# Kernel optimization log

Hardware: AMD Instinct MI355X
Metric: run time of the kernel (lower is better)

The kernel has to match this reference:

```python
import jax, jax.numpy as jnp
from jax import lax
import numpy as np

INPUT, HIDDEN, OUTPUT, SEQ = 1024, 1024, 1024, 8192


def setup_inputs() -> dict:
    key = jax.random.key(0)
    ks = jax.random.split(key, 7)
    s = 1.0 / np.sqrt(HIDDEN)
    return {
        "input_seq": jax.random.normal(ks[0], (SEQ, INPUT), dtype=jnp.float32),
        # PyTorch nn.LSTM params, gate order [i, f, g, o]
        "W_ih": jax.random.uniform(ks[1], (4 * HIDDEN, INPUT), jnp.float32, -s, s),
        "W_hh": jax.random.uniform(ks[2], (4 * HIDDEN, HIDDEN), jnp.float32, -s, s),
        "b_ih": jax.random.uniform(ks[3], (4 * HIDDEN,), jnp.float32, -s, s),
        "b_hh": jax.random.uniform(ks[4], (4 * HIDDEN,), jnp.float32, -s, s),
        "W_out": jax.random.uniform(ks[5], (OUTPUT, HIDDEN), jnp.float32, -s, s),
        "b_out": jax.random.uniform(ks[6], (OUTPUT,), jnp.float32, -s, s),
    }


def reference(input_seq, W_ih, W_hh, b_ih, b_hh, W_out, b_out):
    H = W_hh.shape[1]
    # Precompute input projections for all timesteps in one GEMM: [S, 4H]
    x_gates = input_seq @ W_ih.T + (b_ih + b_hh)

    def step(carry, xg):
        h, c = carry
        gates = xg + h @ W_hh.T                      # [4H]
        i = jax.nn.sigmoid(gates[:H])
        f = jax.nn.sigmoid(gates[H:2 * H])
        g = jnp.tanh(gates[2 * H:3 * H])
        o = jax.nn.sigmoid(gates[3 * H:])
        c = f * c + i * g
        h = o * jnp.tanh(c)
        return (h, c), None

    h0 = jnp.zeros((H,), dtype=input_seq.dtype)
    (h_final, _), _ = lax.scan(step, (h0, h0), x_gates)
    # Original applies linear per-timestep then takes predictions[-1];
    # linear is pointwise in time, so projecting only h_final is identical math.
    return h_final @ W_out.T + b_out
```

## Files before the change

kernel.cpp:

```cpp
#include <hip/hip_runtime.h>
#include <hip/hip_fp16.h>

typedef _Float16 h2v __attribute__((ext_vector_type(2)));

__device__ __forceinline__ float fdot2(unsigned int a, unsigned int b, float c) {
    return __builtin_amdgcn_fdot2(__builtin_bit_cast(h2v, a),
                                  __builtin_bit_cast(h2v, b), c, false);
}

#define SCOPE_AGENT __HIP_MEMORY_SCOPE_AGENT

__global__ __launch_bounds__(256) void k_f2h(const float* __restrict__ src,
                                             __half* __restrict__ dst, int n4) {
    int i = blockIdx.x * 256 + threadIdx.x;
    if (i >= n4) return;
    float4 v = ((const float4*)src)[i];
    union { __half2 h[2]; uint2 u; } o;
    o.h[0] = __halves2half2(__float2half_rn(v.x), __float2half_rn(v.y));
    o.h[1] = __halves2half2(__float2half_rn(v.z), __float2half_rn(v.w));
    ((uint2*)dst)[i] = o.u;
}

__global__ __launch_bounds__(256) void k_bias(const float* __restrict__ a,
                                              const float* __restrict__ b,
                                              float* __restrict__ o) {
    int i = blockIdx.x * 256 + threadIdx.x;
    if (i < 4096) o[i] = a[i] + b[i];
}

__global__ __launch_bounds__(256) void k_gemm_xg(const __half* __restrict__ A,
                                                 const __half* __restrict__ B,
                                                 const float* __restrict__ bias,
                                                 __half* __restrict__ C) {
    __shared__ unsigned int As[128][20];
    __shared__ unsigned int Bs[128][20];
    const int tid = threadIdx.x;
    const int tx = tid & 15, ty = tid >> 4;
    const int m0 = blockIdx.x * 128, n0 = blockIdx.y * 128;
    float acc[8][8];
#pragma unroll
    for (int i = 0; i < 8; ++i)
#pragma unroll
        for (int j = 0; j < 8; ++j) acc[i][j] = 0.f;
    const unsigned int* Ag = (const unsigned int*)(A + (size_t)m0 * 1024);
    const unsigned int* Bg = (const unsigned int*)(B + (size_t)n0 * 1024);
    for (int k0 = 0; k0 < 512; k0 += 16) {
        __syncthreads();
#pragma unroll
        for (int j = 0; j < 2; ++j) {
            int qd = j * 256 + tid;
            int row = qd >> 2;
            int c4 = (qd & 3) << 2;
            uint4 va = *(const uint4*)(Ag + (size_t)row * 512 + k0 + c4);
            uint4 vb = *(const uint4*)(Bg + (size_t)row * 512 + k0 + c4);
            *(uint4*)&As[row][c4] = va;
            *(uint4*)&Bs[row][c4] = vb;
        }
        __syncthreads();
#pragma unroll
        for (int k2 = 0; k2 < 16; k2 += 2) {
            unsigned int a0[8], a1[8], b0[8], b1[8];
#pragma unroll
            for (int i = 0; i < 8; ++i) {
                uint2 v = *(const uint2*)&As[ty + 16 * i][k2];
                a0[i] = v.x; a1[i] = v.y;
            }
#pragma unroll
            for (int j = 0; j < 8; ++j) {
                uint2 v = *(const uint2*)&Bs[tx + 16 * j][k2];
                b0[j] = v.x; b1[j] = v.y;
            }
#pragma unroll
            for (int i = 0; i < 8; ++i)
#pragma unroll
                for (int j = 0; j < 8; ++j) {
                    acc[i][j] = fdot2(a0[i], b0[j], acc[i][j]);
                    acc[i][j] = fdot2(a1[i], b1[j], acc[i][j]);
                }
        }
    }
#pragma unroll
    for (int i = 0; i < 8; ++i) {
        int row = m0 + ty + 16 * i;
#pragma unroll
        for (int j = 0; j < 8; ++j) {
            int col = n0 + tx + 16 * j;
            C[(size_t)row * 4096 + col] = __float2half_rn(acc[i][j] + bias[col]);
        }
    }
}

__global__ __launch_bounds__(512, 1) void k_lstm(const __half* __restrict__ Whh,
                                                 const __half* __restrict__ xg,
                                                 unsigned long long* pub) {
    __shared__ unsigned int hs[2][544];
    const int tid = threadIdx.x;
    const int b = blockIdx.x;
    const int w = tid >> 6, lane = tid & 63;
    const int rho = lane >> 2;
    const int cc = lane & 3;
    const int grow = (rho & 3) * 1024 + b * 32 + 4 * w + (rho >> 2);
    uint4 wr[32];
#pragma unroll
    for (int i = 0; i < 32; ++i)
        wr[i] = *(const uint4*)(Whh + (size_t)grow * 1024 + cc * 256 + i * 8);
    const int soff = (tid >> 6) * 68 + (tid & 63);
    float c_state = 0.f;
    __syncthreads();

    for (int t = 0; t < 8192; ++t) {
        float xv = __half2float(xg[(size_t)t * 4096 + grow]);
        unsigned int d = 0;
        if (t > 0) {
            const unsigned long long* src = pub + (((t - 1) & 1) << 9);
            unsigned long long v = __hip_atomic_load(src + tid, __ATOMIC_RELAXED, SCOPE_AGENT);
            while ((unsigned)(v >> 32) != (unsigned)t) {
                __builtin_amdgcn_s_sleep(1);
                v = __hip_atomic_load(src + tid, __ATOMIC_RELAXED, SCOPE_AGENT);
            }
            d = (unsigned)v;
        }
        const int p = t & 1;
        hs[p][soff] = d;
        __syncthreads();
        float acc = 0.f;
        const unsigned int* hsp = &hs[p][cc * 136];
#pragma unroll
        for (int i = 0; i < 32; ++i) {
            uint4 h4 = *(const uint4*)(hsp + (i >> 4) * 68 + ((i & 15) << 2));
            acc = fdot2(wr[i].x, h4.x, acc);
            acc = fdot2(wr[i].y, h4.y, acc);
            acc = fdot2(wr[i].z, h4.z, acc);
            acc = fdot2(wr[i].w, h4.w, acc);
        }
        acc += __shfl_xor(acc, 1);
        acc += __shfl_xor(acc, 2);
        acc += xv;
        const int base = lane & 48;
        float gi = __shfl(acc, base + 0);
        float gf = __shfl(acc, base + 4);
        float gg = __shfl(acc, base + 8);
        float go = __shfl(acc, base + 12);
        gi = 1.f / (1.f + __expf(-gi));
        gf = 1.f / (1.f + __expf(-gf));
        gg = 2.f / (1.f + __expf(-2.f * gg)) - 1.f;
        go = 1.f / (1.f + __expf(-go));
        c_state = gf * c_state + gi * gg;
        float hval = go * (2.f / (1.f + __expf(-2.f * c_state)) - 1.f);
        float ha = __shfl(hval, (lane & 1) << 5);
        float hb = __shfl(hval, ((lane & 1) << 5) + 16);
        if (lane < 2) {
            union { __half2 h; unsigned int u; } pk;
            pk.h = __halves2half2(__float2half_rn(ha), __float2half_rn(hb));
            unsigned long long val =
                ((unsigned long long)(unsigned)(t + 1) << 32) | pk.u;
            __hip_atomic_store(pub + (p << 9) + b * 16 + w * 2 + lane, val,
                               __ATOMIC_RELAXED, SCOPE_AGENT);
        }
    }
}

__global__ __launch_bounds__(256) void k_proj(unsigned long long* __restrict__ hfin,
                                              const float* __restrict__ Wout,
                                              const float* __restrict__ bout,
                                              float* __restrict__ out) {
    __shared__ float red[256];
    const int o = blockIdx.x, tid = threadIdx.x;
    const float* wr = Wout + (size_t)o * 1024;
    float acc = 0.f;
#pragma unroll
    for (int j = 0; j < 2; ++j) {
        int e = j * 256 + tid;
        unsigned long long v = __hip_atomic_load(hfin + e, __ATOMIC_RELAXED, SCOPE_AGENT);
        union { unsigned int u; __half2 h; } pk; pk.u = (unsigned)v;
        acc += __half2float(__low2half(pk.h)) * wr[2 * e] +
               __half2float(__high2half(pk.h)) * wr[2 * e + 1];
    }
    red[tid] = acc;
    __syncthreads();
    for (int s = 128; s > 0; s >>= 1) {
        if (tid < s) red[tid] += red[tid + s];
        __syncthreads();
    }
    if (tid == 0) out[o] = red[0] + bout[o];
}

extern "C" void kernel_launch(void* const* d_in, const int* in_sizes, int n_in,
                              void* d_out, int out_size, void* d_ws, size_t ws_size,
                              hipStream_t stream) {
    const float* input_seq = (const float*)d_in[0];
    const float* W_ih = (const float*)d_in[1];
    const float* W_hh = (const float*)d_in[2];
    const float* b_ih = (const float*)d_in[3];
    const float* b_hh = (const float*)d_in[4];
    const float* W_out = (const float*)d_in[5];
    const float* b_out = (const float*)d_in[6];
    float* out = (float*)d_out;

    char* ws = (char*)d_ws;
    unsigned long long* pub = (unsigned long long*)ws;
    float* bias = (float*)(ws + 24576);
    __half* Wih_h = (__half*)(ws + 65536);
    __half* Whh_h = (__half*)(ws + 65536 + (size_t)8 * 1024 * 1024);
    __half* in_h  = (__half*)(ws + 65536 + (size_t)16 * 1024 * 1024);
    __half* xg    = (__half*)(ws + 65536 + (size_t)32 * 1024 * 1024);

    hipMemsetAsync(ws, 0, 8192, stream);

    k_f2h<<<8192, 256, 0, stream>>>(input_seq, in_h, 2 * 1024 * 1024);
    k_f2h<<<4096, 256, 0, stream>>>(W_ih, Wih_h, 1024 * 1024);
    k_f2h<<<4096, 256, 0, stream>>>(W_hh, Whh_h, 1024 * 1024);
    k_bias<<<16, 256, 0, stream>>>(b_ih, b_hh, bias);

    dim3 gg(64, 32);
    k_gemm_xg<<<gg, 256, 0, stream>>>(in_h, Wih_h, bias, xg);

    k_lstm<<<32, 512, 0, stream>>>(Whh_h, xg, pub);

    k_proj<<<1024, 256, 0, stream>>>(pub + 512, W_out, b_out, out);
}
```

Baseline: 20.88 ms.

## Publish each hidden value as a 16-bit tag plus half word, drop sleep

Each hidden value now goes out as a 32-bit word holding a 16-bit timestep tag and one fp16 value. Four lanes per wave publish directly, which removes the cross-lane shuffles before the store. Readers poll 64-bit pairs and check both tags, and the s_sleep in the spin loop is gone. This is meant to cut publish latency on the serial recurrence critical path. In exchange it uses system-scope atomics, which may cost more per access, and the 16-bit tag wraps at 65536, which is still safe for 8192 steps.

After: 20.70 ms. No clear change (-0.9%).

```diff
diff --git a/kernel.cpp b/kernel.cpp
--- a/kernel.cpp
+++ b/kernel.cpp
@@ -8,7 +8,7 @@
                                   __builtin_bit_cast(h2v, b), c, false);
 }
 
-#define SCOPE_AGENT __HIP_MEMORY_SCOPE_AGENT
+#define SCOPE_SYS __HIP_MEMORY_SCOPE_SYSTEM
 
 __global__ __launch_bounds__(256) void k_f2h(const float* __restrict__ src,
                                              __half* __restrict__ dst, int n4) {
@@ -92,7 +92,7 @@
 
 __global__ __launch_bounds__(512, 1) void k_lstm(const __half* __restrict__ Whh,
                                                  const __half* __restrict__ xg,
-                                                 unsigned long long* pub) {
+                                                 unsigned int* pub) {
     __shared__ unsigned int hs[2][544];
     const int tid = threadIdx.x;
     const int b = blockIdx.x;
@@ -105,6 +105,7 @@
     for (int i = 0; i < 32; ++i)
         wr[i] = *(const uint4*)(Whh + (size_t)grow * 1024 + cc * 256 + i * 8);
     const int soff = (tid >> 6) * 68 + (tid & 63);
+    const int upub = b * 32 + w * 4 + (lane >> 4);
     float c_state = 0.f;
     __syncthreads();
 
@@ -112,13 +113,16 @@
         float xv = __half2float(xg[(size_t)t * 4096 + grow]);
         unsigned int d = 0;
         if (t > 0) {
-            const unsigned long long* src = pub + (((t - 1) & 1) << 9);
-            unsigned long long v = __hip_atomic_load(src + tid, __ATOMIC_RELAXED, SCOPE_AGENT);
-            while ((unsigned)(v >> 32) != (unsigned)t) {
-                __builtin_amdgcn_s_sleep(1);
-                v = __hip_atomic_load(src + tid, __ATOMIC_RELAXED, SCOPE_AGENT);
+            const unsigned long long* src =
+                (const unsigned long long*)(pub + (((t - 1) & 1) << 10)) + tid;
+            const unsigned tt = (unsigned)t;
+            unsigned long long v = __hip_atomic_load(src, __ATOMIC_RELAXED, SCOPE_SYS);
+            unsigned lo = (unsigned)v, hi = (unsigned)(v >> 32);
+            while ((lo >> 16) != tt || (hi >> 16) != tt) {
+                v = __hip_atomic_load(src, __ATOMIC_RELAXED, SCOPE_SYS);
+                lo = (unsigned)v; hi = (unsigned)(v >> 32);
             }
-            d = (unsigned)v;
+            d = (lo & 0xffffu) | (hi << 16);
         }
         const int p = t & 1;
         hs[p][soff] = d;
@@ -147,20 +151,16 @@
         go = 1.f / (1.f + __expf(-go));
         c_state = gf * c_state + gi * gg;
         float hval = go * (2.f / (1.f + __expf(-2.f * c_state)) - 1.f);
-        float ha = __shfl(hval, (lane & 1) << 5);
-        float hb = __shfl(hval, ((lane & 1) << 5) + 16);
-        if (lane < 2) {
-            union { __half2 h; unsigned int u; } pk;
-            pk.h = __halves2half2(__float2half_rn(ha), __float2half_rn(hb));
-            unsigned long long val =
-                ((unsigned long long)(unsigned)(t + 1) << 32) | pk.u;
-            __hip_atomic_store(pub + (p << 9) + b * 16 + w * 2 + lane, val,
-                               __ATOMIC_RELAXED, SCOPE_AGENT);
-        }
-    }
-}
-
-__global__ __launch_bounds__(256) void k_proj(unsigned long long* __restrict__ hfin,
+        if ((lane & 15) == 0) {
+            unsigned val = ((unsigned)(t + 1) << 16) |
+                           (unsigned)__half_as_ushort(__float2half_rn(hval));
+            __hip_atomic_store(pub + (p << 10) + upub, val,
+                               __ATOMIC_RELAXED, SCOPE_SYS);
+        }
+    }
+}
+
+__global__ __launch_bounds__(256) void k_proj(const unsigned int* __restrict__ hfin,
                                               const float* __restrict__ Wout,
                                               const float* __restrict__ bout,
                                               float* __restrict__ out) {
@@ -169,12 +169,10 @@
     const float* wr = Wout + (size_t)o * 1024;
     float acc = 0.f;
 #pragma unroll
-    for (int j = 0; j < 2; ++j) {
+    for (int j = 0; j < 4; ++j) {
         int e = j * 256 + tid;
-        unsigned long long v = __hip_atomic_load(hfin + e, __ATOMIC_RELAXED, SCOPE_AGENT);
-        union { unsigned int u; __half2 h; } pk; pk.u = (unsigned)v;
-        acc += __half2float(__low2half(pk.h)) * wr[2 * e] +
-               __half2float(__high2half(pk.h)) * wr[2 * e + 1];
+        unsigned v = hfin[e];
+        acc += __half2float(__ushort_as_half((unsigned short)(v & 0xffffu))) * wr[e];
     }
     red[tid] = acc;
     __syncthreads();
@@ -198,7 +196,7 @@
     float* out = (float*)d_out;
 
     char* ws = (char*)d_ws;
-    unsigned long long* pub = (unsigned long long*)ws;
+    unsigned int* pub = (unsigned int*)ws;
     float* bias = (float*)(ws + 24576);
     __half* Wih_h = (__half*)(ws + 65536);
     __half* Whh_h = (__half*)(ws + 65536 + (size_t)8 * 1024 * 1024);
@@ -217,5 +215,5 @@
 
     k_lstm<<<32, 512, 0, stream>>>(Whh_h, xg, pub);
 
-    k_proj<<<1024, 256, 0, stream>>>(pub + 512, W_out, b_out, out);
-}
+    k_proj<<<1024, 256, 0, stream>>>(pub + 1024, W_out, b_out, out);
+}
```
